# Optimization experiments

Hardware: AMD Instinct MI355X
Metric: run time of the kernel (lower is better)

## Reference

```python
import jax, jax.numpy as jnp
import numpy as np


def _parallel_scan_affine(log_a, b):
    """Hillis-Steele doubling scan for h_t = a_t*h_{t-1} + b_t (h_0 = 0).

    log_a, b: (B, T, d). Operator: (la2,b2) o (la1,b1) = (la1+la2, exp(la2)*b1 + b2).
    """
    T = log_a.shape[1]
    la, bv = log_a, b
    stride = 1
    while stride < T:  # static Python loop, log2(T) rounds
        la_prev = jnp.roll(la, stride, axis=1).at[:, :stride, :].set(0.0)
        bv_prev = jnp.roll(bv, stride, axis=1).at[:, :stride, :].set(0.0)
        bv = jnp.exp(la) * bv_prev + bv
        la = la + la_prev
        stride *= 2
    return bv


def setup_inputs() -> dict:
    key = jax.random.key(0)
    kx, kwz, kwh = jax.random.split(key, 3)
    B, T, D = 4, 4096, 1024
    x = jax.random.normal(kx, (B, T, D), dtype=jnp.float32)
    # nn.Linear(D, D) weights, stored as (out, in) like torch
    Wz = jax.random.normal(kwz, (D, D), dtype=jnp.float32) * 0.02
    bz = jnp.zeros((D,), dtype=jnp.float32)
    Wh = jax.random.normal(kwh, (D, D), dtype=jnp.float32) * 0.02
    bh = jnp.zeros((D,), dtype=jnp.float32)
    return {"x": x, "Wz": Wz, "bz": bz, "Wh": Wh, "bh": bh}


def reference(x, Wz, bz, Wh, bh):
    # forward_parallel: z = sigmoid(linear_z(x)); h_tilde = linear_h(x)
    z = jax.nn.sigmoid(jnp.einsum("btd,ed->bte", x, Wz) + bz)
    h_tilde = jnp.einsum("btd,ed->bte", x, Wh) + bh
    log_a = jnp.log(1.0 - z + 1e-08)
    b = z * h_tilde
    h_out = _parallel_scan_affine(log_a, b)
    return h_out  # out_proj is Identity since d_inner == d_model
```

## Files before the change

### kernel.cpp

```cpp
#include <hip/hip_runtime.h>
#include <hip/hip_bf16.h>


typedef __bf16 bf16x8 __attribute__((ext_vector_type(8)));
typedef __bf16 bf16x4 __attribute__((ext_vector_type(4)));
typedef float  f32x4  __attribute__((ext_vector_type(4)));

#define BSZ 4
#define TSZ 4096
#define DSZ 1024
#define MSZ (BSZ*TSZ)
#define CH  16
#define NC  (TSZ/CH)

__device__ __forceinline__ void gload_lds16(const __bf16* g, __bf16* l) {
  __builtin_amdgcn_global_load_lds(
      (const __attribute__((address_space(1))) void*)g,
      (__attribute__((address_space(3))) void*)l, 16, 0, 0);
}

__global__ void convert_tile_kernel(const float* __restrict__ X,
                                    const float* __restrict__ Wz,
                                    const float* __restrict__ Wh,
                                    __bf16* __restrict__ Xc,
                                    __bf16* __restrict__ Wzc,
                                    __bf16* __restrict__ Whc)
{
  const int bx = blockIdx.x;
  const float* src; __bf16* dst; int gid;
  if (bx < 8192)      { src = X;  dst = Xc;  gid =  bx        *256 + threadIdx.x; }
  else if (bx < 8704) { src = Wz; dst = Wzc; gid = (bx - 8192)*256 + threadIdx.x; }
  else                { src = Wh; dst = Whc; gid = (bx - 8704)*256 + threadIdx.x; }
  const int l    = gid & 63;
  const int i    = (gid >> 6) & 7;
  const int kblk = (gid >> 9) & 31;
  const int rblk = gid >> 14;
  const int row  = rblk*128 + i*16 + (l & 15);
  const int col  = kblk*32 + (l >> 4)*8;
  const float* g = src + (size_t)row*DSZ + col;
  float4 v0 = *(const float4*)g;
  float4 v1 = *(const float4*)(g + 4);
  bf16x8 p;
  p[0]=(__bf16)v0.x; p[1]=(__bf16)v0.y; p[2]=(__bf16)v0.z; p[3]=(__bf16)v0.w;
  p[4]=(__bf16)v1.x; p[5]=(__bf16)v1.y; p[6]=(__bf16)v1.z; p[7]=(__bf16)v1.w;
  *(bf16x8*)(dst + (size_t)gid*8) = p;
}

__global__ __launch_bounds__(256, 2) void gemm_gate_kernel(
    const __bf16* __restrict__ Xc,  const __bf16* __restrict__ Wzc,
    const __bf16* __restrict__ Whc,
    const float* __restrict__ bz, const float* __restrict__ bh,
    __bf16* __restrict__ a_ws, float* __restrict__ b_out,
    float* __restrict__ Aprod, float* __restrict__ Bcomp)
{
  __shared__ __align__(16) __bf16 As [8192];
  __shared__ __align__(16) __bf16 Bzs[8192];
  __shared__ __align__(16) __bf16 Bhs[8192];

  const int tid  = threadIdx.x;
  const int lane = tid & 63;
  const int wv   = tid >> 6;
  const int wM   = (wv >> 1) * 64;
  const int wN   = (wv & 1) * 64;
  const int wMg  = wM >> 4;
  const int wNg  = wN >> 4;
  const int lr   = lane & 15;
  const int q    = lane >> 4;
  const int wbase = wv * 64;

  const __bf16* Xb = Xc  + (size_t)blockIdx.x * 32 * 4096;
  const __bf16* Zb = Wzc + (size_t)blockIdx.y * 32 * 4096;
  const __bf16* Hb = Whc + (size_t)blockIdx.y * 32 * 4096;

  f32x4 accz[4][4] = {};
  f32x4 acch[4][4] = {};

  for (int kblk = 0; kblk < 16; ++kblk) {
    __syncthreads();
    const size_t tb = (size_t)kblk * 8192;
    #pragma unroll
    for (int c = 0; c < 4; ++c) {
      const int eo = (c*256 + wbase + lane) * 8;
      const int lo = (c*256 + wbase) * 8;
      gload_lds16(Xb + tb + eo, As  + lo);
      gload_lds16(Zb + tb + eo, Bzs + lo);
      gload_lds16(Hb + tb + eo, Bhs + lo);
    }
    __syncthreads();

    #pragma unroll
    for (int h = 0; h < 2; ++h) {
      const int ho = h * 4096;
      bf16x8 af[4];
      #pragma unroll
      for (int i = 0; i < 4; ++i)
        af[i] = *(const bf16x8*)(As + ho + (wMg + i)*512 + lane*8);
      #pragma unroll
      for (int j = 0; j < 4; ++j) {
        bf16x8 bz8 = *(const bf16x8*)(Bzs + ho + (wNg + j)*512 + lane*8);
        bf16x8 bh8 = *(const bf16x8*)(Bhs + ho + (wNg + j)*512 + lane*8);
        #pragma unroll
        for (int i = 0; i < 4; ++i) {
          accz[j][i] = __builtin_amdgcn_mfma_f32_16x16x32_bf16(af[i], bz8, accz[j][i], 0, 0, 0);
          acch[j][i] = __builtin_amdgcn_mfma_f32_16x16x32_bf16(af[i], bh8, acch[j][i], 0, 0, 0);
        }
      }
    }
  }

  const int M0 = blockIdx.x * 128;
  const int N0 = blockIdx.y * 128;
  #pragma unroll
  for (int j = 0; j < 4; ++j) {
    const int e = N0 + wN + j*16 + lr;
    const float bzv = bz[e];
    const float bhv = bh[e];
    #pragma unroll
    for (int i = 0; i < 4; ++i) {
      const int mbase = M0 + wM + i*16 + q*4;
      float Ar[4], Br[4];
      float A = 1.0f, Bv = 0.0f;
      #pragma unroll
      for (int r = 0; r < 4; ++r) {
        const float pz = accz[j][i][r] + bzv;
        const float ph = acch[j][i][r] + bhv;
        const float ex = __expf(-pz);
        const float z  = 1.0f / (1.0f + ex);
        const float af = (float)(__bf16)fmaf(ex, z, 1e-8f);
        const float bf = z * ph;
        Bv = fmaf(af, Bv, bf);
        A *= af;
        Ar[r] = A; Br[r] = Bv;
      }
      float sA = A, sB = Bv;
      #pragma unroll
      for (int s = 16; s < 64; s <<= 1) {
        const float Ap = __shfl_up(sA, s, 64);
        const float Bp = __shfl_up(sB, s, 64);
        if (lane >= s) { sB = fmaf(sA, Bp, sB); sA *= Ap; }
      }
      float EA = __shfl_up(sA, 16, 64);
      float EB = __shfl_up(sB, 16, 64);
      if (q == 0) { EA = 1.0f; EB = 0.0f; }
      #pragma unroll
      for (int r = 0; r < 4; ++r) {
        const size_t idx = (size_t)(mbase + r)*DSZ + e;
        const float Apre = Ar[r] * EA;
        const float Bpre = fmaf(Ar[r], EB, Br[r]);
        a_ws[idx]  = (__bf16)Apre;
        b_out[idx] = Bpre;
      }
      if (q == 3) {
        const int bc = (M0 + wM + i*16) >> 4;
        Aprod[(size_t)bc*DSZ + e] = sA;
        Bcomp[(size_t)bc*DSZ + e] = sB;
      }
    }
  }
}

#define P2B 16
__global__ void scan_pass2_kernel(const float* Aprod,
                                  const float* __restrict__ Bcomp,
                                  float* Hstart)
{
  const int lane = threadIdx.x & 63;
  const int b    = blockIdx.x >> 4;
  const int d    = (blockIdx.x & 15) * 64 + lane;
  const size_t base = (size_t)b * NC * DSZ + d;
  float h = 0.0f;
  for (int c0 = 0; c0 < NC; c0 += P2B) {
    float Ar[P2B], Br[P2B];
    #pragma unroll
    for (int c = 0; c < P2B; ++c) {
      Ar[c] = Aprod[base + (size_t)(c0 + c)*DSZ];
      Br[c] = Bcomp[base + (size_t)(c0 + c)*DSZ];
    }
    #pragma unroll
    for (int c = 0; c < P2B; ++c) {
      Hstart[base + (size_t)(c0 + c)*DSZ] = h;
      h = fmaf(Ar[c], h, Br[c]);
    }
  }
}

__global__ void scan_pass3_kernel(const __bf16* __restrict__ a_ws,
                                  const float* __restrict__ Hstart,
                                  float* __restrict__ out)
{
  const int bc   = blockIdx.x;
  const int d0   = threadIdx.x * 4;
  const size_t base = (size_t)bc * CH * DSZ + d0;
  const float4 hv = *(const float4*)(Hstart + (size_t)bc*DSZ + d0);
  const float h0[4] = {hv.x, hv.y, hv.z, hv.w};
  #pragma unroll
  for (int t = 0; t < CH; ++t) {
    bf16x4 a4 = *(const bf16x4*)(a_ws + base + (size_t)t*DSZ);
    float4 b4 = *(const float4*)(out + base + (size_t)t*DSZ);
    float o[4] = {b4.x, b4.y, b4.z, b4.w};
    #pragma unroll
    for (int c = 0; c < 4; ++c)
      o[c] = fmaf((float)a4[c], h0[c], o[c]);
    *(float4*)(out + base + (size_t)t*DSZ) = make_float4(o[0], o[1], o[2], o[3]);
  }
}

extern "C" void kernel_launch(void* const* d_in, const int* in_sizes, int n_in,
                              void* d_out, int out_size, void* d_ws, size_t ws_size,
                              hipStream_t stream)
{
  const float* x  = (const float*)d_in[0];
  const float* Wz = (const float*)d_in[1];
  const float* bz = (const float*)d_in[2];
  const float* Wh = (const float*)d_in[3];
  const float* bh = (const float*)d_in[4];
  float* out = (float*)d_out;

  __bf16* Xc   = (__bf16*)d_ws;
  __bf16* Wzc  = Xc  + (size_t)MSZ * DSZ;
  __bf16* Whc  = Wzc + (size_t)DSZ * DSZ;
  __bf16* a_ws = Whc + (size_t)DSZ * DSZ;
  float* Aprod  = (float*)(a_ws + (size_t)MSZ * DSZ);
  float* Bcomp  = Aprod + (size_t)BSZ*NC*DSZ;
  float* Hstart = Aprod;

  convert_tile_kernel<<<9216, 256, 0, stream>>>(x, Wz, Wh, Xc, Wzc, Whc);
  gemm_gate_kernel<<<dim3(MSZ/128, DSZ/128), 256, 0, stream>>>(
      Xc, Wzc, Whc, bz, bh, a_ws, out, Aprod, Bcomp);
  scan_pass2_kernel<<<64, 64, 0, stream>>>(Aprod, Bcomp, Hstart);
  scan_pass3_kernel<<<BSZ*NC, 256, 0, stream>>>(a_ws, Hstart, out);
}
```

Measured before the change: 243.7 us.

## Fuse chunked scan into GEMM epilogue via decoupled look-back across blocks

Drops the two separate scan passes and the bf16 a/b intermediate writes. Each GEMM block publishes its 128-row chunk aggregate and does a decoupled look-back over earlier blocks in the same batch, using atomic flags and a dynamic block-id counter. It then recomputes the gate values and writes the final output once. This removes the workspace round-trip and two kernel launches, at the cost of serialised look-back latency and spin-waiting inside the GEMM.

```diff
diff --git a/kernel.cpp b/kernel.cpp
--- a/kernel.cpp
+++ b/kernel.cpp
@@ -3,7 +3,6 @@
 
 
 typedef __bf16 bf16x8 __attribute__((ext_vector_type(8)));
-typedef __bf16 bf16x4 __attribute__((ext_vector_type(4)));
 typedef float  f32x4  __attribute__((ext_vector_type(4)));
 
 #define BSZ 4
@@ -12,6 +11,8 @@
 #define MSZ (BSZ*TSZ)
 #define CH  16
 #define NC  (TSZ/CH)
+#define CPB 32
+#define NBLK 1024
 
 __device__ __forceinline__ void gload_lds16(const __bf16* g, __bf16* l) {
   __builtin_amdgcn_global_load_lds(
@@ -24,9 +25,15 @@
                                     const float* __restrict__ Wh,
                                     __bf16* __restrict__ Xc,
                                     __bf16* __restrict__ Wzc,
-                                    __bf16* __restrict__ Whc)
+                                    __bf16* __restrict__ Whc,
+                                    int* __restrict__ ctrl)
 {
   const int bx = blockIdx.x;
+  if (bx == 0) {
+    #pragma unroll
+    for (int k = 0; k < 4; ++k) ctrl[k*256 + threadIdx.x] = 0;
+    if (threadIdx.x == 0) ctrl[NBLK] = 0;
+  }
   const float* src; __bf16* dst; int gid;
   if (bx < 8192)      { src = X;  dst = Xc;  gid =  bx        *256 + threadIdx.x; }
   else if (bx < 8704) { src = Wz; dst = Wzc; gid = (bx - 8192)*256 + threadIdx.x; }
@@ -46,18 +53,27 @@
   *(bf16x8*)(dst + (size_t)gid*8) = p;
 }
 
-__global__ __launch_bounds__(256, 2) void gemm_gate_kernel(
+__global__ __launch_bounds__(256, 2) void gemm_scan_kernel(
     const __bf16* __restrict__ Xc,  const __bf16* __restrict__ Wzc,
     const __bf16* __restrict__ Whc,
     const float* __restrict__ bz, const float* __restrict__ bh,
-    __bf16* __restrict__ a_ws, float* __restrict__ b_out,
-    float* __restrict__ Aprod, float* __restrict__ Bcomp)
+    float* __restrict__ out,
+    float* aggA, float* aggB, float* incA, float* incB, int* ctrl)
 {
   __shared__ __align__(16) __bf16 As [8192];
   __shared__ __align__(16) __bf16 Bzs[8192];
   __shared__ __align__(16) __bf16 Bhs[8192];
+  __shared__ int vbid_s;
 
   const int tid  = threadIdx.x;
+  if (tid == 0)
+    vbid_s = __hip_atomic_fetch_add(&ctrl[NBLK], 1, __ATOMIC_RELAXED,
+                                    __HIP_MEMORY_SCOPE_AGENT) & (NBLK - 1);
+  __syncthreads();
+  const int vbid = vbid_s;
+  const int bx = vbid & 127;
+  const int by = vbid >> 7;
+
   const int lane = tid & 63;
   const int wv   = tid >> 6;
   const int wM   = (wv >> 1) * 64;
@@ -66,11 +82,12 @@
   const int wNg  = wN >> 4;
   const int lr   = lane & 15;
   const int q    = lane >> 4;
+  const int wr   = wv >> 1;
   const int wbase = wv * 64;
 
-  const __bf16* Xb = Xc  + (size_t)blockIdx.x * 32 * 4096;
-  const __bf16* Zb = Wzc + (size_t)blockIdx.y * 32 * 4096;
-  const __bf16* Hb = Whc + (size_t)blockIdx.y * 32 * 4096;
+  const __bf16* Xb = Xc  + (size_t)bx * 32 * 4096;
+  const __bf16* Zb = Wzc + (size_t)by * 32 * 4096;
+  const __bf16* Hb = Whc + (size_t)by * 32 * 4096;
 
   f32x4 accz[4][4] = {};
   f32x4 acch[4][4] = {};
@@ -108,8 +125,16 @@
     }
   }
 
-  const int M0 = blockIdx.x * 128;
-  const int N0 = blockIdx.y * 128;
+  const int M0 = bx * 128, N0 = by * 128;
+  const int cb = bx & ~(CPB-1);
+  const int fidx = vbid;
+
+  __syncthreads();
+  float* ldsA = (float*)As;
+  float* ldsB = ldsA + 1024;
+  float* hsL  = ldsB + 1024;
+
+  float EA[4][4], EB[4][4];
   #pragma unroll
   for (int j = 0; j < 4; ++j) {
     const int e = N0 + wN + j*16 + lr;
@@ -117,8 +142,6 @@
     const float bhv = bh[e];
     #pragma unroll
     for (int i = 0; i < 4; ++i) {
-      const int mbase = M0 + wM + i*16 + q*4;
-      float Ar[4], Br[4];
       float A = 1.0f, Bv = 0.0f;
       #pragma unroll
       for (int r = 0; r < 4; ++r) {
@@ -126,11 +149,10 @@
         const float ph = acch[j][i][r] + bhv;
         const float ex = __expf(-pz);
         const float z  = 1.0f / (1.0f + ex);
-        const float af = (float)(__bf16)fmaf(ex, z, 1e-8f);
+        const float af = fmaf(ex, z, 1e-8f);
         const float bf = z * ph;
         Bv = fmaf(af, Bv, bf);
         A *= af;
-        Ar[r] = A; Br[r] = Bv;
       }
       float sA = A, sB = Bv;
       #pragma unroll
@@ -139,69 +161,108 @@
         const float Bp = __shfl_up(sB, s, 64);
         if (lane >= s) { sB = fmaf(sA, Bp, sB); sA *= Ap; }
       }
-      float EA = __shfl_up(sA, 16, 64);
-      float EB = __shfl_up(sB, 16, 64);
-      if (q == 0) { EA = 1.0f; EB = 0.0f; }
+      float eA = __shfl_up(sA, 16, 64);
+      float eB = __shfl_up(sB, 16, 64);
+      if (q == 0) { eA = 1.0f; eB = 0.0f; }
+      EA[j][i] = eA; EB[j][i] = eB;
+      const float cA = __shfl(sA, 48 + lr, 64);
+      const float cB = __shfl(sB, 48 + lr, 64);
+      if (q == 0) {
+        ldsA[(wr*4 + i)*128 + (e - N0)] = cA;
+        ldsB[(wr*4 + i)*128 + (e - N0)] = cB;
+      }
+    }
+  }
+  __syncthreads();
+
+  float bA[4], bB[4];
+  if (wr == 1 && q == 0) {
+    #pragma unroll
+    for (int j = 0; j < 4; ++j) {
+      const int dl = wN + j*16 + lr;
+      float A = 1.0f, Bv = 0.0f;
+      #pragma unroll
+      for (int c = 0; c < 8; ++c) {
+        const float cA = ldsA[c*128 + dl];
+        const float cB = ldsB[c*128 + dl];
+        Bv = fmaf(cA, Bv, cB);
+        A *= cA;
+      }
+      bA[j] = A; bB[j] = Bv;
+      const size_t sidx = (size_t)fidx*128 + dl;
+      __hip_atomic_store(&aggA[sidx], A,  __ATOMIC_RELAXED, __HIP_MEMORY_SCOPE_AGENT);
+      __hip_atomic_store(&aggB[sidx], Bv, __ATOMIC_RELAXED, __HIP_MEMORY_SCOPE_AGENT);
+    }
+  }
+  __syncthreads();
+  if (tid == 0)
+    __hip_atomic_store(&ctrl[fidx], 1, __ATOMIC_RELEASE, __HIP_MEMORY_SCOPE_AGENT);
+
+  if (wr == 1 && q == 0) {
+    float Aex[4] = {1.f,1.f,1.f,1.f}, Bex[4] = {0.f,0.f,0.f,0.f};
+    for (int k = fidx - 1; (k & 127) >= cb && (k & 127) != 127; --k) {
+      int f;
+      do {
+        f = __hip_atomic_load(&ctrl[k], __ATOMIC_ACQUIRE, __HIP_MEMORY_SCOPE_AGENT);
+        f = __builtin_amdgcn_readfirstlane(f);
+        if (f == 0) __builtin_amdgcn_s_sleep(4);
+      } while (f == 0);
+      const float* pA = (f == 2) ? incA : aggA;
+      const float* pB = (f == 2) ? incB : aggB;
+      #pragma unroll
+      for (int j = 0; j < 4; ++j) {
+        const int dl = wN + j*16 + lr;
+        const size_t sidx = (size_t)k*128 + dl;
+        const float kA = __hip_atomic_load(&pA[sidx], __ATOMIC_RELAXED, __HIP_MEMORY_SCOPE_AGENT);
+        const float kB = __hip_atomic_load(&pB[sidx], __ATOMIC_RELAXED, __HIP_MEMORY_SCOPE_AGENT);
+        Bex[j] = fmaf(Aex[j], kB, Bex[j]);
+        Aex[j] *= kA;
+      }
+      if (f == 2) break;
+    }
+    #pragma unroll
+    for (int j = 0; j < 4; ++j) {
+      const int dl = wN + j*16 + lr;
+      const size_t sidx = (size_t)fidx*128 + dl;
+      __hip_atomic_store(&incA[sidx], Aex[j]*bA[j],            __ATOMIC_RELAXED, __HIP_MEMORY_SCOPE_AGENT);
+      __hip_atomic_store(&incB[sidx], fmaf(bA[j],Bex[j],bB[j]),__ATOMIC_RELAXED, __HIP_MEMORY_SCOPE_AGENT);
+      float h = Bex[j];
+      #pragma unroll
+      for (int c = 0; c < 8; ++c) {
+        hsL[c*128 + dl] = h;
+        h = fmaf(ldsA[c*128 + dl], h, ldsB[c*128 + dl]);
+      }
+    }
+  }
+  __syncthreads();
+  if (tid == 0)
+    __hip_atomic_store(&ctrl[fidx], 2, __ATOMIC_RELEASE, __HIP_MEMORY_SCOPE_AGENT);
+
+  #pragma unroll
+  for (int j = 0; j < 4; ++j) {
+    const int e = N0 + wN + j*16 + lr;
+    const float bzv = bz[e];
+    const float bhv = bh[e];
+    #pragma unroll
+    for (int i = 0; i < 4; ++i) {
+      const int mbase = M0 + wM + i*16 + q*4;
+      const float hs = hsL[(wr*4 + i)*128 + (e - N0)];
+      float A = 1.0f, Bv = 0.0f;
       #pragma unroll
       for (int r = 0; r < 4; ++r) {
-        const size_t idx = (size_t)(mbase + r)*DSZ + e;
-        const float Apre = Ar[r] * EA;
-        const float Bpre = fmaf(Ar[r], EB, Br[r]);
-        a_ws[idx]  = (__bf16)Apre;
-        b_out[idx] = Bpre;
-      }
-      if (q == 3) {
-        const int bc = (M0 + wM + i*16) >> 4;
-        Aprod[(size_t)bc*DSZ + e] = sA;
-        Bcomp[(size_t)bc*DSZ + e] = sB;
-      }
-    }
-  }
-}
-
-#define P2B 16
-__global__ void scan_pass2_kernel(const float* Aprod,
-                                  const float* __restrict__ Bcomp,
-                                  float* Hstart)
-{
-  const int lane = threadIdx.x & 63;
-  const int b    = blockIdx.x >> 4;
-  const int d    = (blockIdx.x & 15) * 64 + lane;
-  const size_t base = (size_t)b * NC * DSZ + d;
-  float h = 0.0f;
-  for (int c0 = 0; c0 < NC; c0 += P2B) {
-    float Ar[P2B], Br[P2B];
-    #pragma unroll
-    for (int c = 0; c < P2B; ++c) {
-      Ar[c] = Aprod[base + (size_t)(c0 + c)*DSZ];
-      Br[c] = Bcomp[base + (size_t)(c0 + c)*DSZ];
-    }
-    #pragma unroll
-    for (int c = 0; c < P2B; ++c) {
-      Hstart[base + (size_t)(c0 + c)*DSZ] = h;
-      h = fmaf(Ar[c], h, Br[c]);
-    }
-  }
-}
-
-__global__ void scan_pass3_kernel(const __bf16* __restrict__ a_ws,
-                                  const float* __restrict__ Hstart,
-                                  float* __restrict__ out)
-{
-  const int bc   = blockIdx.x;
-  const int d0   = threadIdx.x * 4;
-  const size_t base = (size_t)bc * CH * DSZ + d0;
-  const float4 hv = *(const float4*)(Hstart + (size_t)bc*DSZ + d0);
-  const float h0[4] = {hv.x, hv.y, hv.z, hv.w};
-  #pragma unroll
-  for (int t = 0; t < CH; ++t) {
-    bf16x4 a4 = *(const bf16x4*)(a_ws + base + (size_t)t*DSZ);
-    float4 b4 = *(const float4*)(out + base + (size_t)t*DSZ);
-    float o[4] = {b4.x, b4.y, b4.z, b4.w};
-    #pragma unroll
-    for (int c = 0; c < 4; ++c)
-      o[c] = fmaf((float)a4[c], h0[c], o[c]);
-    *(float4*)(out + base + (size_t)t*DSZ) = make_float4(o[0], o[1], o[2], o[3]);
+        const float pz = accz[j][i][r] + bzv;
+        const float ph = acch[j][i][r] + bhv;
+        const float ex = __expf(-pz);
+        const float z  = 1.0f / (1.0f + ex);
+        const float af = fmaf(ex, z, 1e-8f);
+        const float bf = z * ph;
+        Bv = fmaf(af, Bv, bf);
+        A *= af;
+        const float Apre = A * EA[j][i];
+        const float Bpre = fmaf(A, EB[j][i], Bv);
+        out[(size_t)(mbase + r)*DSZ + e] = fmaf(Apre, hs, Bpre);
+      }
+    }
   }
 }
 
@@ -219,14 +280,13 @@
   __bf16* Xc   = (__bf16*)d_ws;
   __bf16* Wzc  = Xc  + (size_t)MSZ * DSZ;
   __bf16* Whc  = Wzc + (size_t)DSZ * DSZ;
-  __bf16* a_ws = Whc + (size_t)DSZ * DSZ;
-  float* Aprod  = (float*)(a_ws + (size_t)MSZ * DSZ);
-  float* Bcomp  = Aprod + (size_t)BSZ*NC*DSZ;
-  float* Hstart = Aprod;
-
-  convert_tile_kernel<<<9216, 256, 0, stream>>>(x, Wz, Wh, Xc, Wzc, Whc);
-  gemm_gate_kernel<<<dim3(MSZ/128, DSZ/128), 256, 0, stream>>>(
-      Xc, Wzc, Whc, bz, bh, a_ws, out, Aprod, Bcomp);
-  scan_pass2_kernel<<<64, 64, 0, stream>>>(Aprod, Bcomp, Hstart);
-  scan_pass3_kernel<<<BSZ*NC, 256, 0, stream>>>(a_ws, Hstart, out);
-}
+  float*  aggA = (float*)(Whc + (size_t)DSZ * DSZ);
+  float*  aggB = aggA + (size_t)NBLK*128;
+  float*  incA = aggB + (size_t)NBLK*128;
+  float*  incB = incA + (size_t)NBLK*128;
+  int*    ctrl = (int*)(incB + (size_t)NBLK*128);
+
+  convert_tile_kernel<<<9216, 256, 0, stream>>>(x, Wz, Wh, Xc, Wzc, Whc, ctrl);
+  gemm_scan_kernel<<<dim3(128, 8), 256, 0, stream>>>(
+      Xc, Wzc, Whc, bz, bh, out, aggA, aggB, incA, incB, ctrl);
+}
```

Measured after the change: 369.9 us. 1.52x slower.
